# Kernel optimization log

Measured on AMD Instinct MI355X. Metric: run time of the kernel, lower is better.

The kernel has to match this reference:

```python
import jax, jax.numpy as jnp
import numpy as np

N, T, D, H = 128, 128, 1024, 1024


def setup_inputs() -> dict:
    key = jax.random.key(0)
    ks = jax.random.split(key, 5)
    x = jax.random.normal(ks[0], (N, T, D), dtype=jnp.float32)
    A = jax.random.normal(ks[1], (N, H, 4, 4), dtype=jnp.float32)
    Wx = jax.random.normal(ks[2], (D, 4 * H), dtype=jnp.float32) / np.sqrt(D)
    Wh = jax.random.normal(ks[3], (H, 4 * H), dtype=jnp.float32) / np.sqrt(H)
    Wattn = jax.random.normal(ks[4], (H, 4 * H), dtype=jnp.float32) / np.sqrt(H)
    b = jnp.zeros((4 * H,), dtype=jnp.float32)
    return {"x": x, "A": A, "Wx": Wx, "Wh": Wh, "Wattn": Wattn, "b": b}


def reference(x, A, Wx, Wh, Wattn, b):
    n, t, d = x.shape
    h_dim = A.shape[1]
    scale = 1.0 / (h_dim ** 0.5)
    A_flat = A.reshape(n, h_dim, 16)            # (N, H, 16) flattened 4x4 grid
    h0 = A_flat.mean(axis=2)                    # mean-pooled feature init
    c0 = h0

    def step(carry, xt):
        h, c = carry
        # scaled dot-product attention over the 16 spatial positions
        scores = jnp.einsum('nh,nhp->np', h, A_flat) * scale   # (N, 16)
        w = jax.nn.softmax(scores, axis=-1)
        attn = jnp.einsum('nhp,np->nh', A_flat, w)             # (N, H)
        # fused gate pre-activations
        a = h @ Wh + xt @ Wx + attn @ Wattn + b                # (N, 4H)
        ai, af, ao, ag = jnp.split(a, 4, axis=1)
        i = jax.nn.sigmoid(ai)
        f = jax.nn.sigmoid(af)
        o = jax.nn.sigmoid(ao)
        g = jnp.tanh(ag)
        nc = f * c + i * g
        nh = o * jnp.tanh(nc)
        return (nh, nc), nh

    _, hs = jax.lax.scan(step, (h0, c0), jnp.transpose(x, (1, 0, 2)))
    return jnp.transpose(hs, (1, 0, 2))         # (N, T, H)
```

## Files before the change

### kernel.cpp

```cpp
#include <hip/hip_runtime.h>
#include <hip/hip_bf16.h>


typedef __bf16 bf16x8 __attribute__((ext_vector_type(8)));
typedef float f32x4 __attribute__((ext_vector_type(4)));

__device__ __forceinline__ unsigned short f2bf(float f) {
    unsigned int u = __float_as_uint(f);
    u += 0x7FFFu + ((u >> 16) & 1u);
    return (unsigned short)(u >> 16);
}
__device__ __forceinline__ float bf2f(unsigned short u) {
    return __uint_as_float(((unsigned int)u) << 16);
}
__device__ __forceinline__ float sigf(float x) { return 1.0f / (1.0f + __expf(-x)); }
__device__ __forceinline__ float tanhf_fast(float x) {
    const float t = __expf(-2.0f * fabsf(x));
    const float r = (1.0f - t) / (1.0f + t);
    return copysignf(r, x);
}

__global__ __launch_bounds__(256) void k_build_wtf2(
    const float* __restrict__ Wh, const float* __restrict__ Wx,
    unsigned short* __restrict__ WTf) {
    __shared__ float tile[64][65];
    const int cs2 = blockIdx.x;
    const int kq  = blockIdx.y;
    const int tid = threadIdx.x;
#pragma unroll
    for (int it = 0; it < 16; ++it) {
        int idx = it * 256 + tid;
        int kl = idx >> 6, cl = idx & 63;
        int col = cs2 * 64 + cl;
        int j = (col & 3) * 1024 + (col >> 2);
        int k = kq * 64 + kl;
        tile[kl][cl] = (k < 1024) ? Wh[(size_t)k * 4096 + j]
                                  : Wx[(size_t)(k - 1024) * 4096 + j];
    }
    __syncthreads();
#pragma unroll
    for (int it = 0; it < 2; ++it) {
        int slotid = it * 256 + tid;
        int l   = slotid & 63;
        int cf  = (slotid >> 6) & 1;
        int ksl = (slotid >> 7) & 1;
        int sl  = slotid >> 8;
        int s = cs2 * 2 + sl, ks = kq * 2 + ksl;
        int clocal = sl * 32 + cf * 16 + (l & 15);
        int klocal = ksl * 32 + ((l >> 4) << 3);
        unsigned short v[8];
#pragma unroll
        for (int i = 0; i < 8; ++i) v[i] = f2bf(tile[klocal + i][clocal]);
        *(int4*)&WTf[(size_t)(((s * 64 + ks) * 2 + cf) * 64 + l) * 8] = *(const int4*)v;
    }
}

__global__ __launch_bounds__(256) void k_build_wf(
    const float* __restrict__ W, unsigned short* __restrict__ WF) {
    __shared__ float tile[64][65];
    const int cs2 = blockIdx.x;
    const int kq  = blockIdx.y;
    const int tid = threadIdx.x;
#pragma unroll
    for (int it = 0; it < 16; ++it) {
        int idx = it * 256 + tid;
        int kl = idx >> 6, cl = idx & 63;
        int col = cs2 * 64 + cl;
        int j = (col & 3) * 1024 + (col >> 2);
        int k = kq * 64 + kl;
        tile[kl][cl] = W[(size_t)k * 4096 + j];
    }
    __syncthreads();
#pragma unroll
    for (int it = 0; it < 2; ++it) {
        int slotid = it * 256 + tid;
        int l   = slotid & 63;
        int cf  = (slotid >> 6) & 1;
        int ksl = (slotid >> 7) & 1;
        int sl  = slotid >> 8;
        int s = cs2 * 2 + sl, ks = kq * 2 + ksl;
        int clocal = sl * 32 + cf * 16 + (l & 15);
        int klocal = ksl * 32 + ((l >> 4) << 3);
        unsigned short v[8];
#pragma unroll
        for (int i = 0; i < 8; ++i) v[i] = f2bf(tile[klocal + i][clocal]);
        *(int4*)&WF[(size_t)(((s * 32 + ks) * 2 + cf) * 64 + l) * 8] = *(const int4*)v;
    }
}

__global__ __launch_bounds__(256) void k_pack_at(
    const float* __restrict__ Ag, unsigned short* __restrict__ ATf) {
    __shared__ unsigned short lds[1024][17];
    const int n = blockIdx.x;
    const int tid = threadIdx.x;
#pragma unroll
    for (int it = 0; it < 16; ++it) {
        int idx = it * 256 + tid;
        const float4 v = ((const float4*)(Ag + (size_t)n * 16384))[idx];
        int flat = idx * 4;
        int u = flat >> 4, p = flat & 15;
        lds[u][p + 0] = f2bf(v.x); lds[u][p + 1] = f2bf(v.y);
        lds[u][p + 2] = f2bf(v.z); lds[u][p + 3] = f2bf(v.w);
    }
    __syncthreads();
#pragma unroll
    for (int it = 0; it < 8; ++it) {
        int slot = it * 256 + tid;
        int kc = slot >> 6, l = slot & 63;
        int ubase = kc * 32 + ((l >> 4) << 3);
        int p = l & 15;
        unsigned short v[8];
#pragma unroll
        for (int i = 0; i < 8; ++i) v[i] = lds[ubase + i][p];
        *(int4*)&ATf[((size_t)n * 2048 + slot) * 8] = *(const int4*)v;
    }
}

__global__ __launch_bounds__(512) void k_aw_gemm(
    const unsigned short* __restrict__ ATf, const unsigned short* __restrict__ WAf,
    unsigned short* __restrict__ AW) {
    const int ng = blockIdx.x;
    const int ct = blockIdx.y;
    const int tid = threadIdx.x;
    const int lane = tid & 63, wave = tid >> 6;
    const int s = ct * 4 + (wave >> 1), cf = wave & 1;
    const int n0 = ng * 8;
    f32x4 acc[8] = {};
    const unsigned short* bp = WAf + ((size_t)((s * 32) * 2 + cf) * 64 + lane) * 8;
    const unsigned short* ap = ATf + ((size_t)n0 * 2048 + lane) * 8;
#pragma unroll 4
    for (int kc = 0; kc < 32; ++kc) {
        bf16x8 bf = *(const bf16x8*)(bp + (size_t)kc * 1024);
#pragma unroll
        for (int nn = 0; nn < 8; ++nn) {
            bf16x8 af = *(const bf16x8*)(ap + (size_t)nn * 16384 + (size_t)kc * 512);
            acc[nn] = __builtin_amdgcn_mfma_f32_16x16x32_bf16(af, bf, acc[nn], 0, 0, 0);
        }
    }
    const int col = ct * 128 + wave * 16 + (lane & 15);
    const int prow = (lane >> 4) << 2;
#pragma unroll
    for (int nn = 0; nn < 8; ++nn) {
        ushort4 st = make_ushort4(f2bf(acc[nn][0]), f2bf(acc[nn][1]),
                                  f2bf(acc[nn][2]), f2bf(acc[nn][3]));
        *(ushort4*)&AW[((size_t)(n0 + nn) * 4096 + col) * 16 + prow] = st;
    }
}

__global__ __launch_bounds__(512) void k_build_aw(
    const float* __restrict__ Wattn, const float* __restrict__ Ag,
    unsigned short* __restrict__ AW) {
    extern __shared__ float Alds[];
    const int jt = blockIdx.x;
    const int ng = blockIdx.y;
    const int tid = threadIdx.x;
    const int jl = tid & 127, pg = tid >> 7;
    const int jj = jt * 128 + jl;
    for (int nn = 0; nn < 16; ++nn) {
        const int n = ng * 16 + nn;
        __syncthreads();
#pragma unroll
        for (int q = 0; q < 8; ++q) {
            int idx = q * 512 + tid;
            ((float4*)Alds)[idx] = ((const float4*)(Ag + (size_t)n * 16384))[idx];
        }
        __syncthreads();
        f32x4 acc = {0.f, 0.f, 0.f, 0.f};
#pragma unroll 8
        for (int u = 0; u < 1024; ++u) {
            float wv = Wattn[(size_t)u * 4096 + jj];
            const float4 av = *(const float4*)&Alds[u * 16 + pg * 4];
            acc[0] += wv * av.x; acc[1] += wv * av.y;
            acc[2] += wv * av.z; acc[3] += wv * av.w;
        }
        const int g = jj >> 10, unit = jj & 1023;
        const int cre = unit * 4 + g;
        ushort4 st = make_ushort4(f2bf(acc[0]), f2bf(acc[1]), f2bf(acc[2]), f2bf(acc[3]));
        *(ushort4*)&AW[((size_t)n * 4096 + cre) * 16 + pg * 4] = st;
    }
}

__global__ __launch_bounds__(512) void k_init(
    const float* __restrict__ Ag, float* __restrict__ cst,
    unsigned short* __restrict__ hF0, float* __restrict__ sp) {
    const int n = blockIdx.x;
    const int t = threadIdx.x;
    float contrib[16];
#pragma unroll
    for (int p = 0; p < 16; ++p) contrib[p] = 0.f;
#pragma unroll
    for (int e = 0; e < 2; ++e) {
        const int u = t * 2 + e;
        const float4* ap = (const float4*)&Ag[((size_t)n * 1024 + u) * 16];
        float4 a0 = ap[0], a1 = ap[1], a2 = ap[2], a3 = ap[3];
        float s = a0.x + a0.y + a0.z + a0.w + a1.x + a1.y + a1.z + a1.w +
                  a2.x + a2.y + a2.z + a2.w + a3.x + a3.y + a3.z + a3.w;
        float h0 = s * (1.0f / 16.0f);
        cst[n * 1024 + u] = h0;
        const int rfg = n >> 4, kc = u >> 5, l = (n & 15) | (((u >> 3) & 3) << 4);
        hF0[(size_t)((rfg * 32 + kc) * 64 + l) * 8 + (u & 7)] = f2bf(h0);
        contrib[0]  += h0 * a0.x;  contrib[1]  += h0 * a0.y;
        contrib[2]  += h0 * a0.z;  contrib[3]  += h0 * a0.w;
        contrib[4]  += h0 * a1.x;  contrib[5]  += h0 * a1.y;
        contrib[6]  += h0 * a1.z;  contrib[7]  += h0 * a1.w;
        contrib[8]  += h0 * a2.x;  contrib[9]  += h0 * a2.y;
        contrib[10] += h0 * a2.z;  contrib[11] += h0 * a2.w;
        contrib[12] += h0 * a3.x;  contrib[13] += h0 * a3.y;
        contrib[14] += h0 * a3.z;  contrib[15] += h0 * a3.w;
    }
#pragma unroll
    for (int p = 0; p < 16; ++p) {
        contrib[p] += __shfl_xor(contrib[p], 1);
        contrib[p] += __shfl_xor(contrib[p], 2);
    }
    if ((t & 3) == 0) {
        const int slice = t >> 2;
        float4* dst = (float4*)&sp[(size_t)n * 4096 + slice * 16];
        dst[0] = make_float4(contrib[0], contrib[1], contrib[2], contrib[3]);
        dst[1] = make_float4(contrib[4], contrib[5], contrib[6], contrib[7]);
        dst[2] = make_float4(contrib[8], contrib[9], contrib[10], contrib[11]);
        dst[3] = make_float4(contrib[12], contrib[13], contrib[14], contrib[15]);
    }
    *(float4*)&sp[(size_t)n * 4096 + 2048 + t * 4] = make_float4(0.f, 0.f, 0.f, 0.f);
}

__global__ __launch_bounds__(512) void k_soft(
    const float* __restrict__ spin, float* __restrict__ w_ws,
    const float* __restrict__ x, unsigned short* __restrict__ xf, int ts) {
    __shared__ float sq[8][16];
    const int bid = blockIdx.x;
    const int tid = threadIdx.x;
    const int lane = tid & 63, wave = tid >> 6;
    const int n = bid * 8 + wave;
    f32x4 acc = {0.f, 0.f, 0.f, 0.f};
    const float4* base = (const float4*)(spin + (size_t)n * 4096);
#pragma unroll
    for (int it = 0; it < 16; ++it) {
        const float4 v = base[it * 64 + lane];
        acc[0] += v.x; acc[1] += v.y; acc[2] += v.z; acc[3] += v.w;
    }
#pragma unroll
    for (int m = 4; m <= 32; m <<= 1) {
        acc[0] += __shfl_xor(acc[0], m);
        acc[1] += __shfl_xor(acc[1], m);
        acc[2] += __shfl_xor(acc[2], m);
        acc[3] += __shfl_xor(acc[3], m);
    }
    if (lane < 4) *(f32x4*)&sq[wave][lane * 4] = acc;
    __syncthreads();
    if (lane < 16) {
        const float s = sq[wave][lane] * 0.03125f;
        float mx = s;
#pragma unroll
        for (int m = 1; m < 16; m <<= 1) mx = fmaxf(mx, __shfl_xor(mx, m));
        const float e = __expf(s - mx);
        float se = e;
#pragma unroll
        for (int m = 1; m < 16; m <<= 1) se += __shfl_xor(se, m);
        w_ws[n * 16 + lane] = e / se;
    }
#pragma unroll
    for (int it = 0; it < 2; ++it) {
        const int slot = it * 8192 + bid * 512 + tid;
        const int nn = slot >> 7, js = slot & 127, j0 = js * 8;
        const float4* xp = (const float4*)&x[((size_t)nn * 128 + ts) * 1024 + j0];
        float4 x0 = xp[0], x1 = xp[1];
        unsigned short v[8] = {f2bf(x0.x), f2bf(x0.y), f2bf(x0.z), f2bf(x0.w),
                               f2bf(x1.x), f2bf(x1.y), f2bf(x1.z), f2bf(x1.w)};
        const int rfg = nn >> 4, kc = j0 >> 5, l = (nn & 15) | (((j0 >> 3) & 3) << 4);
        *(int4*)&xf[(size_t)((rfg * 32 + kc) * 64 + l) * 8] = *(const int4*)v;
    }
}

__global__ __launch_bounds__(512, 2) void k_step(
    const unsigned short* __restrict__ WTf, const unsigned short* __restrict__ AW,
    const unsigned short* __restrict__ hFin, unsigned short* __restrict__ hFout,
    const unsigned short* __restrict__ xf,
    const float* __restrict__ w_ws, float* __restrict__ sp,
    float* __restrict__ cst, const float* __restrict__ Ag,
    const float* __restrict__ bias4, float* __restrict__ out, int ts) {
    __shared__ float wlds[128][17];
    const int bid0 = blockIdx.x;
    const int cs16 = (bid0 & 7) * 32 + (bid0 >> 3);
    const int tid = threadIdx.x;
    const int lane = tid & 63, wave = tid >> 6;

#pragma unroll
    for (int it = 0; it < 4; ++it) {
        const int idx = it * 512 + tid;
        wlds[idx >> 4][idx & 15] = w_ws[idx];
    }

    const int lq = lane & 15, hi = lane >> 4;
    const int mycol = cs16 * 16 + lq;
    const int u = mycol >> 2, g = mycol & 3;
    const int r0 = wave * 16 + hi * 4;
    int4 aw0[4], aw1[4];
    float cold[4];
#pragma unroll
    for (int e = 0; e < 4; ++e) {
        const int r = r0 + e;
        const int4* awv = (const int4*)&AW[((size_t)r * 4096 + mycol) * 16];
        aw0[e] = awv[0];
        aw1[e] = awv[1];
        cold[e] = cst[r * 1024 + u];
    }
    const float bias = bias4[g * 1024 + u];
    __syncthreads();

    f32x4 acc2[2] = {};
    {
        const unsigned short* aph = hFin + ((size_t)(wave * 32) * 64 + lane) * 8;
        const unsigned short* apx = xf + ((size_t)(wave * 32) * 64 + lane) * 8;
        const unsigned short* bp = WTf
            + ((size_t)(((cs16 >> 1) * 64) * 2 + (cs16 & 1)) * 64 + lane) * 8;
        bf16x8 ar[8], br[8];
#pragma unroll
        for (int i = 0; i < 8; ++i) {
            ar[i] = *(const bf16x8*)(aph + (size_t)i * 512);
            br[i] = *(const bf16x8*)(bp + (size_t)i * 1024);
        }
#pragma unroll
        for (int kb = 0; kb < 64; ++kb) {
            bf16x8 a = ar[kb & 7], b = br[kb & 7];
            if (kb < 56) {
                const int ks = kb + 8;
                ar[kb & 7] = (ks < 32)
                    ? *(const bf16x8*)(aph + (size_t)ks * 512)
                    : *(const bf16x8*)(apx + (size_t)(ks - 32) * 512);
                br[kb & 7] = *(const bf16x8*)(bp + (size_t)ks * 1024);
            }
            acc2[kb >> 5] = __builtin_amdgcn_mfma_f32_16x16x32_bf16(a, b, acc2[kb >> 5], 0, 0, 0);
        }
    }
    const f32x4 acc = acc2[0] + acc2[1];

    float nhv[4];
#pragma unroll
    for (int e = 0; e < 4; ++e) {
        const int r = r0 + e;
        union { int4 v; unsigned short us[8]; } a0u, a1u;
        a0u.v = aw0[e]; a1u.v = aw1[e];
        float aextra = 0.f;
#pragma unroll
        for (int p = 0; p < 8; ++p) aextra += wlds[r][p] * bf2f(a0u.us[p]);
#pragma unroll
        for (int p = 0; p < 8; ++p) aextra += wlds[r][8 + p] * bf2f(a1u.us[p]);
        float a = acc[e] + bias + aextra;
        float v1 = __shfl_xor(a, 1);
        float v2 = __shfl_xor(a, 2);
        float v3 = __shfl_xor(a, 3);
        auto pick = [&](int m) { return m == 0 ? a : m == 1 ? v1 : m == 2 ? v2 : v3; };
        float ii = sigf(pick(g));
        float ff = sigf(pick(g ^ 1));
        float oo = sigf(pick(g ^ 2));
        float gg = tanhf_fast(pick(g ^ 3));
        const float nc = ff * cold[e] + ii * gg;
        const float nh = oo * tanhf_fast(nc);
        nhv[e] = nh;
        if (g == 0) {
            cst[r * 1024 + u] = nc;
        } else if (g == 1) {
            hFout[(size_t)(((r >> 4) * 32 + (u >> 5)) * 64 +
                           ((r & 15) | (((u >> 3) & 3) << 4))) * 8 + (u & 7)] = f2bf(nh);
        } else if (g == 3) {
            __builtin_nontemporal_store(nh, &out[((size_t)r * 128 + ts) * 1024 + u]);
        }
    }
    if ((lq & 3) == 2) {
#pragma unroll
        for (int e = 0; e < 4; ++e) {
            const int r = r0 + e;
            const float nh = nhv[e];
            const float4* Ap = (const float4*)&Ag[((size_t)r * 1024 + u) * 16];
            float contrib[16];
#pragma unroll
            for (int q = 0; q < 4; ++q) {
                const float4 cv = Ap[q];
                contrib[q * 4 + 0] = nh * cv.x;
                contrib[q * 4 + 1] = nh * cv.y;
                contrib[q * 4 + 2] = nh * cv.z;
                contrib[q * 4 + 3] = nh * cv.w;
            }
#pragma unroll
            for (int p = 0; p < 16; ++p) {
                contrib[p] += __shfl_xor(contrib[p], 4);
                contrib[p] += __shfl_xor(contrib[p], 8);
            }
            if (lq == 2) {
                float4* dst = (float4*)&sp[((size_t)r * 256 + cs16) * 16];
                dst[0] = make_float4(contrib[0], contrib[1], contrib[2], contrib[3]);
                dst[1] = make_float4(contrib[4], contrib[5], contrib[6], contrib[7]);
                dst[2] = make_float4(contrib[8], contrib[9], contrib[10], contrib[11]);
                dst[3] = make_float4(contrib[12], contrib[13], contrib[14], contrib[15]);
            }
        }
    }
}

extern "C" void kernel_launch(void* const* d_in, const int* in_sizes, int n_in,
                              void* d_out, int out_size, void* d_ws, size_t ws_size,
                              hipStream_t stream) {
    const float* x     = (const float*)d_in[0];
    const float* A     = (const float*)d_in[1];
    const float* Wx    = (const float*)d_in[2];
    const float* Wh    = (const float*)d_in[3];
    const float* Wattn = (const float*)d_in[4];
    const float* b     = (const float*)d_in[5];
    float* out = (float*)d_out;

    char* ws = (char*)d_ws;
    unsigned short* WTf = (unsigned short*)(ws);
    unsigned short* AW  = (unsigned short*)(ws + 16777216);
    unsigned short* hF0 = (unsigned short*)(ws + 33554432);
    unsigned short* hF1 = (unsigned short*)(ws + 33816576);
    unsigned short* xf  = (unsigned short*)(ws + 34078720);
    float* cst   = (float*)(ws + 34603008);
    float* w_ws  = (float*)(ws + 35127296);
    float* sp    = (float*)(ws + 35143680);
    unsigned short* ATf = (unsigned short*)(ws + 33554432);
    unsigned short* WAf = (unsigned short*)(ws + 37748736);

    k_build_wtf2<<<dim3(64, 32), 256, 0, stream>>>(Wh, Wx, WTf);
    if (ws_size >= 46137344u) {
        k_build_wf<<<dim3(64, 16), 256, 0, stream>>>(Wattn, WAf);
        k_pack_at<<<128, 256, 0, stream>>>(A, ATf);
        k_aw_gemm<<<dim3(16, 32), 512, 0, stream>>>(ATf, WAf, AW);
    } else {
        k_build_aw<<<dim3(32, 8), 512, 65536, stream>>>(Wattn, A, AW);
    }
    k_init<<<128, 512, 0, stream>>>(A, cst, hF0, sp);

    for (int ts = 0; ts < 128; ++ts) {
        unsigned short* hin  = (ts & 1) ? hF1 : hF0;
        unsigned short* hout = (ts & 1) ? hF0 : hF1;
        k_soft<<<16, 512, 0, stream>>>(sp, w_ws, x, xf, ts);
        k_step<<<256, 512, 0, stream>>>(WTf, AW, hin, hout, xf,
                                        w_ws, sp, cst, A, b, out, ts);
    }
}
```

Before: 3.141 ms.

## Split k_step K-reduction across waves with LDS reduction, 1024-thread blocks

Each block now computes a 64-row by 32-column output tile with 16 waves. Each wave handles half the K dimension (the h part or the x part) and 16 of the 32 columns, and the two partial accumulators are summed through shared memory. This halves the serial MFMA chain per wave (32 instead of 64) and doubles the waves available to hide latency. The cost is an LDS round-trip, a block barrier, and a 1024-thread block whose launch bounds may constrain registers.

New measurement: 2.834 ms. 1.11x faster.

```diff
diff --git a/kernel.cpp b/kernel.cpp
--- a/kernel.cpp
+++ b/kernel.cpp
@@ -272,7 +272,7 @@
     }
 }
 
-__global__ __launch_bounds__(512, 2) void k_step(
+__global__ __launch_bounds__(1024, 4) void k_step(
     const unsigned short* __restrict__ WTf, const unsigned short* __restrict__ AW,
     const unsigned short* __restrict__ hFin, unsigned short* __restrict__ hFout,
     const unsigned short* __restrict__ xf,
@@ -280,65 +280,68 @@
     float* __restrict__ cst, const float* __restrict__ Ag,
     const float* __restrict__ bias4, float* __restrict__ out, int ts) {
     __shared__ float wlds[128][17];
+    __shared__ f32x4 accred[16][64];
     const int bid0 = blockIdx.x;
-    const int cs16 = (bid0 & 7) * 32 + (bid0 >> 3);
+    const int lid = (bid0 & 7) * 32 + (bid0 >> 3);
+    const int cs32 = lid >> 1, rh = lid & 1;
     const int tid = threadIdx.x;
     const int lane = tid & 63, wave = tid >> 6;
-
-#pragma unroll
-    for (int it = 0; it < 4; ++it) {
-        const int idx = it * 512 + tid;
+    const int rf = wave >> 2, kh = (wave >> 1) & 1, cf = wave & 1;
+
+#pragma unroll
+    for (int it = 0; it < 2; ++it) {
+        const int idx = it * 1024 + tid;
         wlds[idx >> 4][idx & 15] = w_ws[idx];
     }
 
+    f32x4 acc = {0.f, 0.f, 0.f, 0.f};
+    {
+        const unsigned short* ap = (kh == 0 ? hFin : xf)
+            + ((size_t)((rh * 4 + rf) * 32) * 64 + lane) * 8;
+        const unsigned short* bp = WTf
+            + ((size_t)(((cs32 * 64 + kh * 32) * 2) + cf) * 64 + lane) * 8;
+        bf16x8 ar[8], br[8];
+#pragma unroll
+        for (int i = 0; i < 8; ++i) {
+            ar[i] = *(const bf16x8*)(ap + (size_t)i * 512);
+            br[i] = *(const bf16x8*)(bp + (size_t)i * 1024);
+        }
+#pragma unroll
+        for (int kb = 0; kb < 32; ++kb) {
+            bf16x8 a = ar[kb & 7], b = br[kb & 7];
+            if (kb < 24) {
+                ar[kb & 7] = *(const bf16x8*)(ap + (size_t)(kb + 8) * 512);
+                br[kb & 7] = *(const bf16x8*)(bp + (size_t)(kb + 8) * 1024);
+            }
+            acc = __builtin_amdgcn_mfma_f32_16x16x32_bf16(a, b, acc, 0, 0, 0);
+        }
+    }
+
     const int lq = lane & 15, hi = lane >> 4;
-    const int mycol = cs16 * 16 + lq;
+    const int mycol = cs32 * 32 + cf * 16 + lq;
     const int u = mycol >> 2, g = mycol & 3;
-    const int r0 = wave * 16 + hi * 4;
-    int4 aw0[4], aw1[4];
-    float cold[4];
-#pragma unroll
-    for (int e = 0; e < 4; ++e) {
-        const int r = r0 + e;
+    const int r0 = rh * 64 + rf * 16 + hi * 4;
+    int4 aw0[2], aw1[2];
+    float cold[2];
+#pragma unroll
+    for (int e = 0; e < 2; ++e) {
+        const int r = r0 + kh * 2 + e;
         const int4* awv = (const int4*)&AW[((size_t)r * 4096 + mycol) * 16];
         aw0[e] = awv[0];
         aw1[e] = awv[1];
         cold[e] = cst[r * 1024 + u];
     }
     const float bias = bias4[g * 1024 + u];
+
+    accred[wave][lane] = acc;
     __syncthreads();
-
-    f32x4 acc2[2] = {};
-    {
-        const unsigned short* aph = hFin + ((size_t)(wave * 32) * 64 + lane) * 8;
-        const unsigned short* apx = xf + ((size_t)(wave * 32) * 64 + lane) * 8;
-        const unsigned short* bp = WTf
-            + ((size_t)(((cs16 >> 1) * 64) * 2 + (cs16 & 1)) * 64 + lane) * 8;
-        bf16x8 ar[8], br[8];
-#pragma unroll
-        for (int i = 0; i < 8; ++i) {
-            ar[i] = *(const bf16x8*)(aph + (size_t)i * 512);
-            br[i] = *(const bf16x8*)(bp + (size_t)i * 1024);
-        }
-#pragma unroll
-        for (int kb = 0; kb < 64; ++kb) {
-            bf16x8 a = ar[kb & 7], b = br[kb & 7];
-            if (kb < 56) {
-                const int ks = kb + 8;
-                ar[kb & 7] = (ks < 32)
-                    ? *(const bf16x8*)(aph + (size_t)ks * 512)
-                    : *(const bf16x8*)(apx + (size_t)(ks - 32) * 512);
-                br[kb & 7] = *(const bf16x8*)(bp + (size_t)ks * 1024);
-            }
-            acc2[kb >> 5] = __builtin_amdgcn_mfma_f32_16x16x32_bf16(a, b, acc2[kb >> 5], 0, 0, 0);
-        }
-    }
-    const f32x4 acc = acc2[0] + acc2[1];
-
-    float nhv[4];
-#pragma unroll
-    for (int e = 0; e < 4; ++e) {
-        const int r = r0 + e;
+    acc += accred[wave ^ 2][lane];
+
+    float nhv[2];
+#pragma unroll
+    for (int e = 0; e < 2; ++e) {
+        const int reg = kh * 2 + e;
+        const int r = r0 + reg;
         union { int4 v; unsigned short us[8]; } a0u, a1u;
         a0u.v = aw0[e]; a1u.v = aw1[e];
         float aextra = 0.f;
@@ -346,7 +349,7 @@
         for (int p = 0; p < 8; ++p) aextra += wlds[r][p] * bf2f(a0u.us[p]);
 #pragma unroll
         for (int p = 0; p < 8; ++p) aextra += wlds[r][8 + p] * bf2f(a1u.us[p]);
-        float a = acc[e] + bias + aextra;
+        float a = acc[reg] + bias + aextra;
         float v1 = __shfl_xor(a, 1);
         float v2 = __shfl_xor(a, 2);
         float v3 = __shfl_xor(a, 3);
@@ -369,8 +372,8 @@
     }
     if ((lq & 3) == 2) {
 #pragma unroll
-        for (int e = 0; e < 4; ++e) {
-            const int r = r0 + e;
+        for (int e = 0; e < 2; ++e) {
+            const int r = r0 + kh * 2 + e;
             const float nh = nhv[e];
             const float4* Ap = (const float4*)&Ag[((size_t)r * 1024 + u) * 16];
             float contrib[16];
@@ -388,7 +391,7 @@
                 contrib[p] += __shfl_xor(contrib[p], 8);
             }
             if (lq == 2) {
-                float4* dst = (float4*)&sp[((size_t)r * 256 + cs16) * 16];
+                float4* dst = (float4*)&sp[((size_t)r * 256 + (cs32 * 2 + cf)) * 16];
                 dst[0] = make_float4(contrib[0], contrib[1], contrib[2], contrib[3]);
                 dst[1] = make_float4(contrib[4], contrib[5], contrib[6], contrib[7]);
                 dst[2] = make_float4(contrib[8], contrib[9], contrib[10], contrib[11]);
@@ -435,7 +438,7 @@
         unsigned short* hin  = (ts & 1) ? hF1 : hF0;
         unsigned short* hout = (ts & 1) ? hF0 : hF1;
         k_soft<<<16, 512, 0, stream>>>(sp, w_ws, x, xf, ts);
-        k_step<<<256, 512, 0, stream>>>(WTf, AW, hin, hout, xf,
-                                        w_ws, sp, cst, A, b, out, ts);
-    }
-}
+        k_step<<<256, 1024, 0, stream>>>(WTf, AW, hin, hout, xf,
+                                         w_ws, sp, cst, A, b, out, ts);
+    }
+}
```
